# Kernel tuning notes

Hardware: AMD Instinct MI355X
Metric: run time of the kernel (lower is better)

The kernel has to match this reference:

```python
import jax, jax.numpy as jnp
import numpy as np

B, T, IN, OUT = 8, 2048, 2048, 2048

def setup_inputs() -> dict:
    key = jax.random.key(0)
    k1, k2, k3, k4 = jax.random.split(key, 4)
    x = jax.random.normal(k1, (B, T, IN), dtype=jnp.float32)
    # ternary weights in {-1, 0, 1}, stored as int8 like the torch buffer
    w_q = (jax.random.randint(k2, (OUT, IN), 0, 3) - 1).astype(jnp.int8)
    # per-output-channel power-of-two exponents (downscaling), int8 buffer
    s_exp = jax.random.randint(k3, (OUT,), -8, 1).astype(jnp.int8)
    bias = jax.random.normal(k4, (OUT,), dtype=jnp.float32) * 0.1
    return {"x": x, "w_q": w_q, "s_exp": s_exp, "bias": bias}

def reference(x, w_q, s_exp, bias):
    # F.linear(x, w_q.float()): y[b,t,o] = sum_i x[b,t,i] * w_q[o,i]
    y = jnp.einsum('bti,oi->bto', x, w_q.astype(x.dtype))
    # torch.ldexp(y, s_exp): y * 2**s_exp, broadcast over last dim
    y = y * jnp.exp2(s_exp.astype(jnp.float32)).astype(x.dtype)
    return y + bias
```

## Files before the change

kernel.cpp:

```cpp
#include <hip/hip_runtime.h>

#define MT 16384
#define NT 2048
#define KT 2048
#define BM 256
#define BN 256
#define BK 64
#define NKT (KT / BK)
#define THREADS 512

typedef __attribute__((ext_vector_type(8))) short short8;
typedef __attribute__((ext_vector_type(4))) float f32x4;
typedef __attribute__((ext_vector_type(8))) unsigned short ushort8;
typedef __attribute__((ext_vector_type(4))) unsigned short ushort4v;

__device__ __forceinline__ unsigned short f32_bf16(float f) {
    union { float f; unsigned u; } v; v.f = f;
    return (unsigned short)((v.u + 0x7FFFu + ((v.u >> 16) & 1u)) >> 16);
}


__global__ __launch_bounds__(256) void cvt_kernel(const float* __restrict__ x,
                                                  const int* __restrict__ w,
                                                  unsigned short* __restrict__ xb,
                                                  unsigned short* __restrict__ wb) {
    const int b = blockIdx.x;
    if (b < MT * KT / 2048) {
        size_t i = ((size_t)b * 256 + threadIdx.x) * 8;
        float4 v0 = *(const float4*)(x + i);
        float4 v1 = *(const float4*)(x + i + 4);
        ushort8 o;
        o[0] = f32_bf16(v0.x); o[1] = f32_bf16(v0.y); o[2] = f32_bf16(v0.z); o[3] = f32_bf16(v0.w);
        o[4] = f32_bf16(v1.x); o[5] = f32_bf16(v1.y); o[6] = f32_bf16(v1.z); o[7] = f32_bf16(v1.w);
        *(ushort8*)(xb + i) = o;
    } else {
        size_t i = ((size_t)(b - MT * KT / 2048) * 256 + threadIdx.x) * 8;
        int4 v0 = *(const int4*)(w + i);
        int4 v1 = *(const int4*)(w + i + 4);
        ushort8 o;
        o[0] = f32_bf16((float)v0.x); o[1] = f32_bf16((float)v0.y);
        o[2] = f32_bf16((float)v0.z); o[3] = f32_bf16((float)v0.w);
        o[4] = f32_bf16((float)v1.x); o[5] = f32_bf16((float)v1.y);
        o[6] = f32_bf16((float)v1.z); o[7] = f32_bf16((float)v1.w);
        *(ushort8*)(wb + i) = o;
    }
}


__global__ __launch_bounds__(THREADS, 2) void gemm_8ph(
    const unsigned short* __restrict__ Abf, const unsigned short* __restrict__ Bbf,
    const int* __restrict__ sexp, const float* __restrict__ bias,
    float* __restrict__ C)
{
    __shared__ unsigned short As[2 * 2048 * 8];
    __shared__ unsigned short Bs[2 * 2048 * 8];

    const int tid  = threadIdx.x;
    const int bn   = blockIdx.x;
    const int bm   = blockIdx.y;
    const int brow0 = bm * BM;
    const int bcol0 = bn * BN;
    const int lane = tid & 63;
    const int wave = tid >> 6;
    const int wm = wave >> 2;
    const int wn = wave & 3;
    const int q = lane >> 4, r = lane & 15;

    size_t aoff[2][2], boff[2][2];
    #pragma unroll
    for (int h = 0; h < 2; ++h)
        #pragma unroll
        for (int ii = 0; ii < 2; ++ii) {
            const int s   = h * 1024 + ii * 512 + tid;
            const int row = s >> 3;
            const int cg  = ((s & 7) - row) & 7;
            aoff[h][ii] = (size_t)(brow0 + row) * KT + cg * 8;
            boff[h][ii] = (size_t)(bcol0 + row) * KT + cg * 8;
        }

#define GLDS(srcp, dstp)                                                            \
    __builtin_amdgcn_global_load_lds(                                               \
        (const __attribute__((address_space(1))) unsigned int*)(srcp),              \
        (__attribute__((address_space(3))) unsigned int*)(dstp), 16, 0, 0)

    auto stageA = [&](int tile, int h) {
        const int buf = tile & 1;
        const size_t k = (size_t)tile * BK;
        GLDS(Abf + aoff[h][0] + k, As + buf * 16384 + (h * 1024 + wave * 64) * 8);
        GLDS(Abf + aoff[h][1] + k, As + buf * 16384 + (h * 1024 + 512 + wave * 64) * 8);
    };
    auto stageB = [&](int tile, int h) {
        const int buf = tile & 1;
        const size_t k = (size_t)tile * BK;
        GLDS(Bbf + boff[h][0] + k, Bs + buf * 16384 + (h * 1024 + wave * 64) * 8);
        GLDS(Bbf + boff[h][1] + k, Bs + buf * 16384 + (h * 1024 + 512 + wave * 64) * 8);
    };

    f32x4 acc[8][4] = {};
    short8 a[4];
    short8 b[4];

    auto ldA = [&](int buf, int fq, int kh) {
        const unsigned short* base = As + buf * 16384;
        #pragma unroll
        for (int u = 0; u < 4; ++u) {
            const int row = (2 * (fq * 4 + u) + wm) * 16 + r;
            a[u] = *(const short8*)(base + row * 64 + ((kh * 4 + q + row) & 7) * 8);
        }
    };
    auto ldB = [&](int buf, int kh) {
        const unsigned short* base = Bs + buf * 16384;
        #pragma unroll
        for (int j = 0; j < 4; ++j) {
            const int row = wn * 64 + j * 16 + r;
            b[j] = *(const short8*)(base + row * 64 + ((kh * 4 + q + row) & 7) * 8);
        }
    };
    auto mma = [&](int fq) {
        #pragma unroll
        for (int u = 0; u < 4; ++u)
            #pragma unroll
            for (int j = 0; j < 4; ++j)
                acc[fq * 4 + u][j] = __builtin_amdgcn_mfma_f32_16x16x32_bf16(
                    a[u], b[j], acc[fq * 4 + u][j], 0, 0, 0);
    };

#define PHASE(buf, fq, kh, STAGE_STMT, WAIT_STMT) do {     \
        ldA(buf, fq, kh);                                  \
        if ((fq) == 0) ldB(buf, kh);                       \
        STAGE_STMT;                                        \
        __builtin_amdgcn_s_barrier();                      \
        asm volatile("s_waitcnt lgkmcnt(0)");              \
        __builtin_amdgcn_sched_barrier(0);                 \
        __builtin_amdgcn_s_setprio(1);                     \
        mma(fq);                                           \
        __builtin_amdgcn_s_setprio(0);                     \
        WAIT_STMT;                                         \
        __builtin_amdgcn_s_barrier();                      \
    } while (0)

#define TILE(buf, t, PH0_STAGE, PH3_STAGE, PH3_WAIT) do {  \
        PHASE(buf, 0, 0, PH0_STAGE, (void)0);              \
        PHASE(buf, 1, 0, (void)0,   (void)0);              \
        PHASE(buf, 0, 1, (void)0,   (void)0);              \
        PHASE(buf, 1, 1, PH3_STAGE, PH3_WAIT);             \
    } while (0)

    stageB(0, 0); stageB(0, 1); stageA(0, 0); stageA(0, 1);
    stageB(1, 0); stageB(1, 1); stageA(1, 0);
    asm volatile("s_waitcnt vmcnt(6)" ::: "memory");
    __builtin_amdgcn_s_barrier();

    #pragma unroll 1
    for (int i = 0; i < 15; ++i) {
        const int t0 = 2 * i, t1 = 2 * i + 1;
        TILE(0, t0,
             { stageA(t0 + 1, 1); },
             { stageB(t0 + 2, 0); stageB(t0 + 2, 1); stageA(t0 + 2, 0); },
             asm volatile("s_waitcnt vmcnt(6)" ::: "memory"));
        TILE(1, t1,
             { stageA(t1 + 1, 1); },
             { stageB(t1 + 2, 0); stageB(t1 + 2, 1); stageA(t1 + 2, 0); },
             asm volatile("s_waitcnt vmcnt(6)" ::: "memory"));
    }

    TILE(0, 30,
         { stageA(31, 1); },
         (void)0,
         asm volatile("s_waitcnt vmcnt(0)" ::: "memory"));
    TILE(1, 31, (void)0, (void)0, (void)0);

#undef TILE
#undef PHASE
#undef GLDS

    #pragma unroll
    for (int j = 0; j < 4; ++j) {
        const int n  = bcol0 + wn * 64 + j * 16 + r;
        const float sc = ldexpf(1.0f, sexp[n]);
        const float bs = bias[n];
        #pragma unroll
        for (int f = 0; f < 8; ++f) {
            const int m = brow0 + (2 * f + wm) * 16 + q * 4;
            float* cp = C + (size_t)m * NT + n;
            #pragma unroll
            for (int t = 0; t < 4; ++t)
                cp[(size_t)t * NT] = acc[f][j][t] * sc + bs;
        }
    }
}


__device__ __forceinline__ int swzf(int row, int c) { return row * 8 + ((c + row) & 7); }

__global__ __launch_bounds__(256) void gemm_fb(
    const float* __restrict__ Af32, const int* __restrict__ Wi32,
    const int* __restrict__ sexp, const float* __restrict__ bias,
    float* __restrict__ C)
{
    __shared__ unsigned short As[128 * 64];
    __shared__ unsigned short Bs[128 * 64];

    const int tid  = threadIdx.x;
    const int row0 = blockIdx.y * 128;
    const int col0 = blockIdx.x * 128;
    const int lane = tid & 63;
    const int wave = tid >> 6;
    const int wm = wave >> 1, wn = wave & 1;
    const int q = lane >> 4, r = lane & 15;

    f32x4 acc[4][4] = {};

    for (int k0 = 0; k0 < KT; k0 += 64) {
        #pragma unroll
        for (int ii = 0; ii < 8; ++ii) {
            const int s  = tid + ii * 256;
            const int rw = s >> 4, c4 = s & 15;
            const int ch = c4 >> 1, hf = c4 & 1;
            const int ps = ((ch + rw) & 7) * 8 + hf * 4;
            float4 v = *(const float4*)(Af32 + (size_t)(row0 + rw) * KT + k0 + c4 * 4);
            ushort4v oa;
            oa[0] = f32_bf16(v.x); oa[1] = f32_bf16(v.y);
            oa[2] = f32_bf16(v.z); oa[3] = f32_bf16(v.w);
            *(ushort4v*)(As + rw * 64 + ps) = oa;
            int4 w4 = *(const int4*)(Wi32 + (size_t)(col0 + rw) * KT + k0 + c4 * 4);
            ushort4v ob;
            ob[0] = f32_bf16((float)w4.x); ob[1] = f32_bf16((float)w4.y);
            ob[2] = f32_bf16((float)w4.z); ob[3] = f32_bf16((float)w4.w);
            *(ushort4v*)(Bs + rw * 64 + ps) = ob;
        }
        __syncthreads();
        #pragma unroll
        for (int h = 0; h < 2; ++h) {
            short8 a[4], b[4];
            #pragma unroll
            for (int i = 0; i < 4; ++i)
                a[i] = *(const short8*)(As + swzf(wm * 64 + i * 16 + r, h * 4 + q) * 8);
            #pragma unroll
            for (int j = 0; j < 4; ++j)
                b[j] = *(const short8*)(Bs + swzf(wn * 64 + j * 16 + r, h * 4 + q) * 8);
            #pragma unroll
            for (int i = 0; i < 4; ++i)
                #pragma unroll
                for (int j = 0; j < 4; ++j)
                    acc[i][j] = __builtin_amdgcn_mfma_f32_16x16x32_bf16(a[i], b[j], acc[i][j], 0, 0, 0);
        }
        __syncthreads();
    }

    #pragma unroll
    for (int j = 0; j < 4; ++j) {
        const int n  = col0 + wn * 64 + j * 16 + r;
        const float sc = ldexpf(1.0f, sexp[n]);
        const float bs = bias[n];
        #pragma unroll
        for (int i = 0; i < 4; ++i) {
            const int m = row0 + wm * 64 + i * 16 + q * 4;
            float* cp = C + (size_t)m * NT + n;
            #pragma unroll
            for (int t = 0; t < 4; ++t)
                cp[(size_t)t * NT] = acc[i][j][t] * sc + bs;
        }
    }
}

extern "C" void kernel_launch(void* const* d_in, const int* in_sizes, int n_in,
                              void* d_out, int out_size, void* d_ws, size_t ws_size,
                              hipStream_t stream) {
    const float* x    = (const float*)d_in[0];
    const int*   wq   = (const int*)d_in[1];
    const int*   se   = (const int*)d_in[2];
    const float* bias = (const float*)d_in[3];
    float* out = (float*)d_out;

    const size_t xb_elems = (size_t)MT * KT;
    const size_t wb_elems = (size_t)NT * KT;

    if (ws_size >= (xb_elems + wb_elems) * sizeof(unsigned short)) {
        unsigned short* xb = (unsigned short*)d_ws;
        unsigned short* wb = xb + xb_elems;
        cvt_kernel<<<(int)((xb_elems + wb_elems) / (256 * 8)), 256, 0, stream>>>(x, wq, xb, wb);
        dim3 grid(NT / BN, MT / BM);
        gemm_8ph<<<grid, THREADS, 0, stream>>>(xb, wb, se, bias, out);
    } else {
        dim3 fgrid(NT / 128, MT / 128);
        gemm_fb<<<fgrid, 256, 0, stream>>>(x, wq, se, bias, out);
    }
}
```

Baseline: 370.0 us.

## Reorder GEMM main loop into quadrant phases with full-K fragments and spread staging

Restructures the per-tile schedule so each phase loads A and B fragments for both K halves and computes one 128x32 quadrant of the warp's output. This lets fragments be reused across phases: the last phase reuses already-loaded registers and issues no LDS reads. The global-to-LDS staging loads are spread one per phase rather than bunched in the last phase, and the prologue issue order changes to match. The intent is fewer LDS reads per MFMA and smoother overlap of global loads, at the cost of more fragment registers and a different dependency pattern between A/B buffers and barriers.

```diff
diff --git a/kernel.cpp b/kernel.cpp
--- a/kernel.cpp
+++ b/kernel.cpp
@@ -97,81 +97,106 @@
     };
 
     f32x4 acc[8][4] = {};
-    short8 a[4];
-    short8 b[4];
-
-    auto ldA = [&](int buf, int fq, int kh) {
+    short8 af[4][2];
+    short8 bf0[2][2];
+    short8 bf1[2][2];
+
+    auto ldA = [&](int buf, int fq) {
         const unsigned short* base = As + buf * 16384;
         #pragma unroll
         for (int u = 0; u < 4; ++u) {
             const int row = (2 * (fq * 4 + u) + wm) * 16 + r;
-            a[u] = *(const short8*)(base + row * 64 + ((kh * 4 + q + row) & 7) * 8);
-        }
-    };
-    auto ldB = [&](int buf, int kh) {
+            #pragma unroll
+            for (int kh = 0; kh < 2; ++kh)
+                af[u][kh] = *(const short8*)(base + row * 64 + ((kh * 4 + q + row) & 7) * 8);
+        }
+    };
+    auto ldB = [&](int buf, int bh, short8 (&bf)[2][2]) {
         const unsigned short* base = Bs + buf * 16384;
         #pragma unroll
-        for (int j = 0; j < 4; ++j) {
-            const int row = wn * 64 + j * 16 + r;
-            b[j] = *(const short8*)(base + row * 64 + ((kh * 4 + q + row) & 7) * 8);
-        }
-    };
-    auto mma = [&](int fq) {
+        for (int v = 0; v < 2; ++v) {
+            const int row = wn * 64 + (bh * 2 + v) * 16 + r;
+            #pragma unroll
+            for (int kh = 0; kh < 2; ++kh)
+                bf[v][kh] = *(const short8*)(base + row * 64 + ((kh * 4 + q + row) & 7) * 8);
+        }
+    };
+    auto mma = [&](int fq, int bh, short8 (&bf)[2][2]) {
         #pragma unroll
         for (int u = 0; u < 4; ++u)
             #pragma unroll
-            for (int j = 0; j < 4; ++j)
-                acc[fq * 4 + u][j] = __builtin_amdgcn_mfma_f32_16x16x32_bf16(
-                    a[u], b[j], acc[fq * 4 + u][j], 0, 0, 0);
-    };
-
-#define PHASE(buf, fq, kh, STAGE_STMT, WAIT_STMT) do {     \
-        ldA(buf, fq, kh);                                  \
-        if ((fq) == 0) ldB(buf, kh);                       \
-        STAGE_STMT;                                        \
-        __builtin_amdgcn_s_barrier();                      \
-        asm volatile("s_waitcnt lgkmcnt(0)");              \
-        __builtin_amdgcn_sched_barrier(0);                 \
-        __builtin_amdgcn_s_setprio(1);                     \
-        mma(fq);                                           \
-        __builtin_amdgcn_s_setprio(0);                     \
-        WAIT_STMT;                                         \
-        __builtin_amdgcn_s_barrier();                      \
+            for (int v = 0; v < 2; ++v)
+                #pragma unroll
+                for (int kh = 0; kh < 2; ++kh)
+                    acc[fq * 4 + u][bh * 2 + v] = __builtin_amdgcn_mfma_f32_16x16x32_bf16(
+                        af[u][kh], bf[v][kh], acc[fq * 4 + u][bh * 2 + v], 0, 0, 0);
+    };
+
+#define BARRIER()   __builtin_amdgcn_s_barrier()
+#define LGKM0()     do { asm volatile("s_waitcnt lgkmcnt(0)");                 \
+                         __builtin_amdgcn_sched_barrier(0); } while (0)
+#define PRIO(x)     __builtin_amdgcn_s_setprio(x)
+
+#define TILE(buf, S0, S1, S2, S3, W3) do {                                     \
+                                                  \
+        ldA(buf, 0); ldB(buf, 0, bf0);                                         \
+        S0;                                                                    \
+        asm volatile("s_waitcnt lgkmcnt(8)");      \
+        BARRIER(); LGKM0();                                                    \
+        PRIO(1); mma(0, 0, bf0); PRIO(0);                                      \
+        BARRIER();                                                             \
+                                                   \
+        ldB(buf, 1, bf1);                                                      \
+        S1;                                                                    \
+        BARRIER(); LGKM0();                                                    \
+        PRIO(1); mma(0, 1, bf1); PRIO(0);                                      \
+        BARRIER();                                                             \
+                                                   \
+        ldA(buf, 1);                                                           \
+        S2;                                                                    \
+        BARRIER(); LGKM0();                                                    \
+        PRIO(1); mma(1, 1, bf1); PRIO(0);                                      \
+        BARRIER();                                                             \
+            \
+        S3;                                                                    \
+        BARRIER();                                                             \
+        PRIO(1); mma(1, 0, bf0); PRIO(0);                                      \
+        W3;                                                                    \
+        BARRIER();                                                             \
     } while (0)
 
-#define TILE(buf, t, PH0_STAGE, PH3_STAGE, PH3_WAIT) do {  \
-        PHASE(buf, 0, 0, PH0_STAGE, (void)0);              \
-        PHASE(buf, 1, 0, (void)0,   (void)0);              \
-        PHASE(buf, 0, 1, (void)0,   (void)0);              \
-        PHASE(buf, 1, 1, PH3_STAGE, PH3_WAIT);             \
-    } while (0)
-
-    stageB(0, 0); stageB(0, 1); stageA(0, 0); stageA(0, 1);
-    stageB(1, 0); stageB(1, 1); stageA(1, 0);
+    stageA(0, 0); stageA(0, 1); stageB(0, 0); stageB(0, 1);
+    stageA(1, 0); stageB(1, 0); stageB(1, 1);
     asm volatile("s_waitcnt vmcnt(6)" ::: "memory");
     __builtin_amdgcn_s_barrier();
 
     #pragma unroll 1
     for (int i = 0; i < 15; ++i) {
         const int t0 = 2 * i, t1 = 2 * i + 1;
-        TILE(0, t0,
+        TILE(0,
              { stageA(t0 + 1, 1); },
-             { stageB(t0 + 2, 0); stageB(t0 + 2, 1); stageA(t0 + 2, 0); },
+             { stageA(t0 + 2, 0); },
+             { stageB(t0 + 2, 0); },
+             { stageB(t0 + 2, 1); },
              asm volatile("s_waitcnt vmcnt(6)" ::: "memory"));
-        TILE(1, t1,
+        TILE(1,
              { stageA(t1 + 1, 1); },
-             { stageB(t1 + 2, 0); stageB(t1 + 2, 1); stageA(t1 + 2, 0); },
+             { stageA(t1 + 2, 0); },
+             { stageB(t1 + 2, 0); },
+             { stageB(t1 + 2, 1); },
              asm volatile("s_waitcnt vmcnt(6)" ::: "memory"));
     }
 
-    TILE(0, 30,
+    TILE(0,
          { stageA(31, 1); },
-         (void)0,
+         (void)0, (void)0, (void)0,
          asm volatile("s_waitcnt vmcnt(0)" ::: "memory"));
-    TILE(1, 31, (void)0, (void)0, (void)0);
+    TILE(1, (void)0, (void)0, (void)0, (void)0, (void)0);
 
 #undef TILE
-#undef PHASE
+#undef PRIO
+#undef LGKM0
+#undef BARRIER
 #undef GLDS
 
     #pragma unroll
```

New measurement: 366.9 us. Within noise of the previous version (-0.8%).
